# Performance work log

Measured on AMD Instinct MI355X. Metric: run time of the kernel, lower is better.

## Reference

```python
import jax, jax.numpy as jnp
import numpy as np
import math

# batch, in-channels, attention_maps, heads, features (== input height), frames
B, C, M, H, F_, W = 2, 8, 8, 8, 256, 512
HD = F_ // H  # head dim = 32


def conv2d(x, w, pad):
    return jax.lax.conv_general_dilated(x, w, (1, 1), pad,
                                        dimension_numbers=('NCHW', 'OIHW', 'NCHW'))


def rotary(x):
    # lucidrains-style interleaved rotary over last dim; x: [..., seq, d]
    d, seq = x.shape[-1], x.shape[-2]
    inv_freq = 1.0 / (10000.0 ** (jnp.arange(0, d, 2, dtype=jnp.float32) / d))
    freqs = jnp.arange(seq, dtype=jnp.float32)[:, None] * inv_freq[None, :]  # [seq, d/2]
    freqs = jnp.repeat(freqs, 2, axis=-1)  # [seq, d], each freq repeated for the (x1,x2) pair
    cos, sin = jnp.cos(freqs), jnp.sin(freqs)
    x1, x2 = x[..., 0::2], x[..., 1::2]
    xr = jnp.stack((-x2, x1), axis=-1).reshape(x.shape)  # rotate_half
    return x * cos + xr * sin


def setup_inputs() -> dict:
    key = jax.random.key(0)
    ks = jax.random.split(key, 12)
    s = 0.02
    return {
        'x': jax.random.normal(ks[0], (B, C, F_, W), jnp.float32),
        'prev_qk': jax.random.normal(ks[1], (B, M, H, W, W), jnp.float32) * 0.1,
        'q_c1': jax.random.normal(ks[2], (M, C, 3, 3), jnp.float32) * s,
        'q_lin': jax.random.normal(ks[3], (M, F_, F_), jnp.float32) * s,
        'q_c2': jax.random.normal(ks[4], (M, M, 1, 3), jnp.float32) * s,
        'k_c1': jax.random.normal(ks[5], (M, C, 3, 3), jnp.float32) * s,
        'k_lin': jax.random.normal(ks[6], (M, F_, F_), jnp.float32) * s,
        'k_c2': jax.random.normal(ks[7], (M, M, 1, 3), jnp.float32) * s,
        'v_c1': jax.random.normal(ks[8], (M, C, 3, 3), jnp.float32) * s,
        'v_lin': jax.random.normal(ks[9], (M, F_, F_), jnp.float32) * s,
        'v_c2': jax.random.normal(ks[10], (M, M, 1, 3), jnp.float32) * s,
        'o_w': jax.random.normal(ks[11], (M, F_, F_), jnp.float32) * s,
    }


def _proj(x, wc1, wl, wc2):
    h = conv2d(x, wc1, [(1, 1), (1, 1)])        # [B,M,F,W] 3x3 conv, no bias
    h = jnp.einsum('bcfw,cgf->bcgw', h, wl)      # MultichannelLinear: per-map linear on feature dim
    h = conv2d(h, wc2, [(0, 0), (1, 1)])         # (1,3) conv along frames
    return h


def _heads(t):
    # [B,M,F,W] -> transpose(2,3) -> [B,M,W,F] -> [B,M,W,H,HD] -> [B,M,H,W,HD]
    return t.transpose(0, 1, 3, 2).reshape(B, M, W, H, HD).transpose(0, 1, 3, 2, 4)


def reference(x, prev_qk, q_c1, q_lin, q_c2, k_c1, k_lin, k_c2, v_c1, v_lin, v_c2, o_w):
    q = rotary(_heads(_proj(x, q_c1, q_lin, q_c2)))
    k = rotary(_heads(_proj(x, k_c1, k_lin, k_c2)))
    v = _heads(_proj(x, v_c1, v_lin, v_c2))
    # scaled by sqrt(h) where h == input height == features (non-standard)
    qk = jnp.einsum('bmhqd,bmhkd->bmhqk', q, k) / math.sqrt(F_) + prev_qk
    a = jnp.einsum('bmhqk,bmhkd->bmhqd', jax.nn.softmax(qk, axis=-1), v)
    a = a.transpose(0, 1, 3, 2, 4).reshape(B, M, W, F_).transpose(0, 1, 3, 2)  # [B,M,F,W]
    out = jnp.einsum('bcfw,cgf->bcgw', a, o_w)  # o_proj MultichannelLinear
    return (out, qk)
```

## Files before the change

kernel.cpp:

```cpp
#include <hip/hip_runtime.h>

#define B 2
#define C 8
#define M 8
#define H 8
#define F 256
#define W 512
#define HD 32
#define MFF (M * F * F)

typedef __attribute__((ext_vector_type(8))) __bf16 bf16x8;
typedef __attribute__((ext_vector_type(4))) float f32x4;

__device__ __forceinline__ unsigned short f2bf(float f) {
    unsigned int u = __float_as_uint(f);
    return (unsigned short)((u + 0x7fffu + ((u >> 16) & 1u)) >> 16);
}

__device__ __forceinline__ unsigned int packsplit(float v) {
    unsigned short h = f2bf(v);
    float hf = __uint_as_float((unsigned int)h << 16);
    unsigned short lo = f2bf(v - hf);
    return (unsigned int)h | ((unsigned int)lo << 16);
}

__global__ __launch_bounds__(256) void wsplit_kernel(const float* __restrict__ w0,
                                                     const float* __restrict__ w1,
                                                     const float* __restrict__ w2,
                                                     const float* __restrict__ w3,
                                                     unsigned short* __restrict__ hi) {
    int idx = blockIdx.x * 256 + threadIdx.x;
    int set = idx >> 17;
    int off = (idx & 131071) * 4;
    const float* src = (set == 0) ? w0 : (set == 1) ? w1 : (set == 2) ? w2 : w3;
    float4 v = *(const float4*)&src[off];
    unsigned short* hp = hi + (size_t)set * MFF + off;
    unsigned short* lp = hp + 4 * MFF;
    ushort4 hv, lv;
    float x;
    x = v.x; hv.x = f2bf(x); lv.x = f2bf(x - __uint_as_float((unsigned)hv.x << 16));
    x = v.y; hv.y = f2bf(x); lv.y = f2bf(x - __uint_as_float((unsigned)hv.y << 16));
    x = v.z; hv.z = f2bf(x); lv.z = f2bf(x - __uint_as_float((unsigned)hv.z << 16));
    x = v.w; hv.w = f2bf(x); lv.w = f2bf(x - __uint_as_float((unsigned)hv.w << 16));
    *(ushort4*)hp = hv;
    *(ushort4*)lp = lv;
}

__global__ __launch_bounds__(256) void conv1_kernel(const float* __restrict__ x,
                                                    const float* __restrict__ w0,
                                                    const float* __restrict__ w1,
                                                    const float* __restrict__ w2,
                                                    unsigned int* __restrict__ out) {
    int t = threadIdx.x;
    int zb = blockIdx.z;
    int b = zb >> 3, m = zb & 7;
    int wi = blockIdx.x * 64 + (t & 63);
    int f0t = blockIdx.y * 32 + (t >> 6) * 8;
    const float* xb = x + (size_t)b * C * F * W;
    const float* wq = w0 + m * 72;
    const float* wk = w1 + m * 72;
    const float* wv = w2 + m * 72;
    int wm = (wi > 0) ? wi - 1 : 0;
    int wp = (wi < W - 1) ? wi + 1 : W - 1;
    bool e0 = (wi > 0), e1 = (wi < W - 1);
    float acc[3][8] = {};
    for (int i = 0; i < 8; ++i) {
        const float* xi = xb + (size_t)i * F * W;
        float v0[10], v1[10], v2[10];
        #pragma unroll
        for (int rr = 0; rr < 10; ++rr) {
            int ff = f0t + rr - 1;
            if (ff >= 0 && ff < F) {
                const float* xr = xi + (size_t)ff * W;
                float a = xr[wm], bb = xr[wi], c = xr[wp];
                v0[rr] = e0 ? a : 0.f;
                v1[rr] = bb;
                v2[rr] = e1 ? c : 0.f;
            } else {
                v0[rr] = 0.f; v1[rr] = 0.f; v2[rr] = 0.f;
            }
        }
        #pragma unroll
        for (int p = 0; p < 3; ++p) {
            const float* wt = ((p == 0) ? wq : (p == 1) ? wk : wv) + i * 9;
            #pragma unroll
            for (int df = 0; df < 3; ++df) {
                float s0 = wt[df * 3 + 0];
                float s1 = wt[df * 3 + 1];
                float s2 = wt[df * 3 + 2];
                #pragma unroll
                for (int ff = 0; ff < 8; ++ff)
                    acc[p][ff] += v0[ff + df] * s0 + v1[ff + df] * s1 + v2[ff + df] * s2;
            }
        }
    }
    #pragma unroll
    for (int p = 0; p < 3; ++p) {
        size_t zo = (size_t)(p * 16 + zb) * F;
        #pragma unroll
        for (int ff = 0; ff < 8; ++ff)
            out[(zo + f0t + ff) * W + wi] = packsplit(acc[p][ff]);
    }
}

__global__ __launch_bounds__(256) void lin_kernel(const unsigned int* __restrict__ in32,
                                                  const unsigned short* __restrict__ whA,
                                                  const unsigned short* __restrict__ whB,
                                                  const unsigned short* __restrict__ whC,
                                                  float* __restrict__ out) {
    __shared__ unsigned int BsH[64][20];
    __shared__ unsigned int BsL[64][20];
    int t = threadIdx.x;
    int z = blockIdx.z;
    int proj = z >> 4, m = z & 7;
    const unsigned short* wh = ((proj == 0) ? whA : (proj == 1) ? whB : whC) + (size_t)m * F * F;
    const unsigned short* wl = wh + 4 * MFF;
    const unsigned int* ib = in32 + (size_t)z * F * W;
    float* ob = out + (size_t)z * F * W;
    int g0 = blockIdx.y * 64, wb0 = blockIdx.x * 64;
    int wv = t >> 6, l = t & 63, lr = l & 15, lg = l >> 4;
    int wgr = wv >> 1, wgc = wv & 1;
    int sp = t & 15;
    int sg = t >> 4;

    uint4 ra, rb;
    ra = *(const uint4*)&ib[(size_t)(2 * sp) * W + wb0 + sg * 4];
    rb = *(const uint4*)&ib[(size_t)(2 * sp + 1) * W + wb0 + sg * 4];

    f32x4 acc[2][2];
    acc[0][0] = (f32x4)0.f; acc[0][1] = (f32x4)0.f;
    acc[1][0] = (f32x4)0.f; acc[1][1] = (f32x4)0.f;

    for (int s = 0; s < 8; ++s) {
        int f0 = s * 32;
        if (s) __syncthreads();
        unsigned int aw[4] = {ra.x, ra.y, ra.z, ra.w};
        unsigned int bw[4] = {rb.x, rb.y, rb.z, rb.w};
        #pragma unroll
        for (int j = 0; j < 4; ++j) {
            BsH[sg * 4 + j][sp] = (aw[j] & 0xFFFFu) | (bw[j] << 16);
            BsL[sg * 4 + j][sp] = (aw[j] >> 16) | (bw[j] & 0xFFFF0000u);
        }
        __syncthreads();
        if (s < 7) {
            ra = *(const uint4*)&ib[(size_t)(f0 + 32 + 2 * sp) * W + wb0 + sg * 4];
            rb = *(const uint4*)&ib[(size_t)(f0 + 32 + 2 * sp + 1) * W + wb0 + sg * 4];
        }
        bf16x8 ah[2], al[2], bh[2], bl[2];
        #pragma unroll
        for (int ti = 0; ti < 2; ++ti) {
            size_t ar = (size_t)(g0 + wgr * 32 + ti * 16 + lr) * F + f0 + lg * 8;
            ah[ti] = *(const bf16x8*)&wh[ar];
            al[ti] = *(const bf16x8*)&wl[ar];
        }
        #pragma unroll
        for (int tj = 0; tj < 2; ++tj) {
            int wc = wgc * 32 + tj * 16 + lr;
            bh[tj] = *(const bf16x8*)((const unsigned short*)&BsH[wc][0] + lg * 8);
            bl[tj] = *(const bf16x8*)((const unsigned short*)&BsL[wc][0] + lg * 8);
        }
        #pragma unroll
        for (int ti = 0; ti < 2; ++ti)
            #pragma unroll
            for (int tj = 0; tj < 2; ++tj) {
                acc[ti][tj] = __builtin_amdgcn_mfma_f32_16x16x32_bf16(ah[ti], bh[tj], acc[ti][tj], 0, 0, 0);
                acc[ti][tj] = __builtin_amdgcn_mfma_f32_16x16x32_bf16(ah[ti], bl[tj], acc[ti][tj], 0, 0, 0);
                acc[ti][tj] = __builtin_amdgcn_mfma_f32_16x16x32_bf16(al[ti], bh[tj], acc[ti][tj], 0, 0, 0);
            }
    }
    #pragma unroll
    for (int ti = 0; ti < 2; ++ti)
        #pragma unroll
        for (int tj = 0; tj < 2; ++tj)
            #pragma unroll
            for (int r = 0; r < 4; ++r) {
                int g = g0 + wgr * 32 + ti * 16 + lg * 4 + r;
                int w = wb0 + wgc * 32 + tj * 16 + lr;
                ob[(size_t)g * W + w] = acc[ti][tj][r];
            }
}

__global__ __launch_bounds__(256) void conv2_heads_kernel(const float* __restrict__ in,
                                                          const float* __restrict__ w0c,
                                                          const float* __restrict__ w1c,
                                                          const float* __restrict__ w2c,
                                                          unsigned short* __restrict__ outp) {
    __shared__ float wl[192];
    __shared__ float Ot[64][65];
    int t = threadIdx.x;
    int z = blockIdx.z;
    int proj = z >> 4, bz = z & 15;
    int b = bz >> 3, o = bz & 7;
    const float* wt = (proj == 0) ? w0c : (proj == 1) ? w1c : w2c;
    int do_rot = (proj < 2);
    if (t < 192) wl[t] = wt[t];
    __syncthreads();
    int f0 = blockIdx.y * 64, w0 = blockIdx.x * 64;
    const float* ib = in + ((size_t)proj * 16 + (size_t)b * M) * F * W;
    int wgi = t & 15, fr = t >> 4;
    int wq = w0 + wgi * 4;
    bool eL = (wq > 0);
    bool eR = (wq + 4 < W);
    #pragma unroll
    for (int fi = 0; fi < 4; ++fi) {
        int f = f0 + fr * 4 + fi;
        float a0 = 0.f, a1 = 0.f, a2 = 0.f, a3 = 0.f;
        #pragma unroll
        for (int i = 0; i < 8; ++i) {
            const float* r = ib + ((size_t)i * F + f) * W + wq;
            float4 v = *(const float4*)r;
            float vlft = eL ? r[-1] : 0.f;
            float vrgt = eR ? r[4] : 0.f;
            const float* wr = &wl[(o * 8 + i) * 3];
            float c0 = wr[0], c1 = wr[1], c2 = wr[2];
            a0 += vlft * c0 + v.x * c1 + v.y * c2;
            a1 += v.x  * c0 + v.y * c1 + v.z * c2;
            a2 += v.y  * c0 + v.z * c1 + v.w * c2;
            a3 += v.z  * c0 + v.w * c1 + vrgt * c2;
        }
        Ot[fr * 4 + fi][wgi * 4 + 0] = a0;
        Ot[fr * 4 + fi][wgi * 4 + 1] = a1;
        Ot[fr * 4 + fi][wgi * 4 + 2] = a2;
        Ot[fr * 4 + fi][wgi * 4 + 3] = a3;
    }
    __syncthreads();
    size_t zbase = (size_t)z * H * W * HD;
    if (do_rot) {
        for (int k = 0; k < 16; ++k) {
            int idx = k * 256 + t;
            int ddh = idx & 63;
            int wi = idx >> 6;
            int f = f0 + ddh;
            int h = f >> 5, d = f & 31;
            float e  = Ot[ddh & ~1][wi];
            float od = Ot[ddh | 1][wi];
            int jp = d >> 1;
            float invf = exp2f(-(float)jp * 0.83048202372184058f);
            float th = (float)(w0 + wi) * invf;
            float cs = __cosf(th), sn = __sinf(th);
            float val = (d & 1) ? (od * cs + e * sn) : (e * cs - od * sn);
            outp[zbase + ((size_t)h * W + (w0 + wi)) * HD + d] = f2bf(val);
        }
    } else {
        for (int k = 0; k < 16; ++k) {
            int idx = k * 256 + t;
            int wi = idx & 63;
            int ddh = idx >> 6;
            int f = f0 + ddh;
            int h = f >> 5, d = f & 31;
            outp[zbase + ((size_t)(h * HD + d)) * W + (w0 + wi)] = f2bf(Ot[ddh][wi]);
        }
    }
}

__global__ __launch_bounds__(256) void attn_kernel(const unsigned short* __restrict__ qb,
                                                   const unsigned short* __restrict__ kb,
                                                   const unsigned short* __restrict__ vtb,
                                                   const float* __restrict__ prev,
                                                   float* __restrict__ qk,
                                                   unsigned int* __restrict__ abuf) {
    __shared__ __align__(16) unsigned short PT[4][16 * 72];
    int t = threadIdx.x;
    int l = t & 63, wv = t >> 6;
    int lr = l & 15, lg = l >> 4;
    int w0 = blockIdx.x * 64;
    int bmh = blockIdx.y;
    const unsigned short* Q  = qb  + (size_t)bmh * W * HD;
    const unsigned short* K  = kb  + (size_t)bmh * W * HD;
    const unsigned short* VT = vtb + (size_t)bmh * HD * W;
    const float* P0 = prev + (size_t)bmh * W * W;
    float* QK = qk + (size_t)bmh * W * W;
    int bm = bmh >> 3, h = bmh & 7;
    unsigned int* A = abuf + ((size_t)bm * F + h * HD) * W;

    int qrow = w0 + wv * 16;
    bf16x8 qf = *(const bf16x8*)&Q[(size_t)(qrow + lr) * HD + lg * 8];

    float m_i[4], l_i[4];
    f32x4 accA[2];
    #pragma unroll
    for (int r = 0; r < 4; ++r) { m_i[r] = -3.0e38f; l_i[r] = 0.f; }
    accA[0] = (f32x4)0.f;
    accA[1] = (f32x4)0.f;

    bf16x8 kfA[4], kfB[4];
    f32x4 pvA[4], pvB[4];

    auto issue = [&](bf16x8 (&kf)[4], f32x4 (&pv)[4], int c) {
        int j0 = c * 64;
        #pragma unroll
        for (int ct = 0; ct < 4; ++ct)
            kf[ct] = *(const bf16x8*)&K[(size_t)(j0 + ct * 16 + lr) * HD + lg * 8];
        #pragma unroll
        for (int ct = 0; ct < 4; ++ct) {
            const float* pr = &P0[(size_t)(qrow + lg * 4) * W + j0 + ct * 16 + lr];
            #pragma unroll
            for (int r = 0; r < 4; ++r) pv[ct][r] = __builtin_nontemporal_load(&pr[(size_t)r * W]);
        }
    };

    auto step = [&](bf16x8 (&kf)[4], f32x4 (&pv)[4], int c) {
        int j0 = c * 64;
        f32x4 sc[4];
        #pragma unroll
        for (int ct = 0; ct < 4; ++ct)
            sc[ct] = __builtin_amdgcn_mfma_f32_16x16x32_bf16(qf, kf[ct], pv[ct] * 16.f, 0, 0, 0);
        bf16x8 vf[2][2];
        #pragma unroll
        for (int ks = 0; ks < 2; ++ks)
            #pragma unroll
            for (int ct2 = 0; ct2 < 2; ++ct2)
                vf[ks][ct2] = *(const bf16x8*)&VT[(size_t)(ct2 * 16 + lr) * W + j0 + ks * 32 + lg * 8];
        float sv[4][4];
        #pragma unroll
        for (int ct = 0; ct < 4; ++ct) {
            #pragma unroll
            for (int r = 0; r < 4; ++r) {
                sv[ct][r] = sc[ct][r] * 0.0625f;
                __builtin_nontemporal_store(sv[ct][r],
                    &QK[(size_t)(qrow + lg * 4 + r) * W + j0 + ct * 16 + lr]);
            }
        }
        float p[4][4];
        #pragma unroll
        for (int r = 0; r < 4; ++r) {
            float cm = fmaxf(fmaxf(sv[0][r], sv[1][r]), fmaxf(sv[2][r], sv[3][r]));
            #pragma unroll
            for (int off = 1; off < 16; off <<= 1) cm = fmaxf(cm, __shfl_xor(cm, off));
            float mn = fmaxf(m_i[r], cm);
            float alpha = __expf(m_i[r] - mn);
            m_i[r] = mn;
            float rs = 0.f;
            #pragma unroll
            for (int ct = 0; ct < 4; ++ct) { p[ct][r] = __expf(sv[ct][r] - mn); rs += p[ct][r]; }
            #pragma unroll
            for (int off = 1; off < 16; off <<= 1) rs += __shfl_xor(rs, off);
            l_i[r] = l_i[r] * alpha + rs;
            accA[0][r] *= alpha;
            accA[1][r] *= alpha;
        }
        unsigned short* PTw = &PT[wv][0];
        #pragma unroll
        for (int ct = 0; ct < 4; ++ct)
            #pragma unroll
            for (int r = 0; r < 4; ++r)
                PTw[(lg * 4 + r) * 72 + ct * 16 + lr] = f2bf(p[ct][r]);
        asm volatile("s_waitcnt lgkmcnt(0)" ::: "memory");
        __builtin_amdgcn_sched_barrier(0);
        bf16x8 pf[2];
        pf[0] = *(const bf16x8*)&PTw[lr * 72 + lg * 8];
        pf[1] = *(const bf16x8*)&PTw[lr * 72 + 32 + lg * 8];
        #pragma unroll
        for (int ks = 0; ks < 2; ++ks)
            #pragma unroll
            for (int ct2 = 0; ct2 < 2; ++ct2)
                accA[ct2] = __builtin_amdgcn_mfma_f32_16x16x32_bf16(pf[ks], vf[ks][ct2], accA[ct2], 0, 0, 0);
    };

    issue(kfA, pvA, 0);
    #pragma unroll
    for (int cc = 0; cc < 4; ++cc) {
        issue(kfB, pvB, 2 * cc + 1);
        step(kfA, pvA, 2 * cc);
        if (cc < 3) issue(kfA, pvA, 2 * cc + 2);
        step(kfB, pvB, 2 * cc + 1);
    }

    float inv[4];
    #pragma unroll
    for (int r = 0; r < 4; ++r) inv[r] = 1.f / l_i[r];
    float* Otf = (float*)&PT[wv][0];
    asm volatile("s_waitcnt lgkmcnt(0)" ::: "memory");
    #pragma unroll
    for (int ct2 = 0; ct2 < 2; ++ct2)
        #pragma unroll
        for (int r = 0; r < 4; ++r)
            Otf[(lg * 4 + r) * 33 + ct2 * 16 + lr] = accA[ct2][r] * inv[r];
    asm volatile("s_waitcnt lgkmcnt(0)" ::: "memory");
    __builtin_amdgcn_sched_barrier(0);
    #pragma unroll
    for (int k = 0; k < 8; ++k) {
        int flat = k * 64 + l;
        int woff = flat & 15, d = flat >> 4;
        A[(size_t)d * W + w0 + wv * 16 + woff] = packsplit(Otf[woff * 33 + d]);
    }
}

extern "C" void kernel_launch(void* const* d_in, const int* in_sizes, int n_in,
                              void* d_out, int out_size, void* d_ws, size_t ws_size,
                              hipStream_t stream) {
    const float* x    = (const float*)d_in[0];
    const float* prev = (const float*)d_in[1];
    const float* qc1  = (const float*)d_in[2];
    const float* qlin = (const float*)d_in[3];
    const float* qc2  = (const float*)d_in[4];
    const float* kc1  = (const float*)d_in[5];
    const float* klin = (const float*)d_in[6];
    const float* kc2  = (const float*)d_in[7];
    const float* vc1  = (const float*)d_in[8];
    const float* vlin = (const float*)d_in[9];
    const float* vc2  = (const float*)d_in[10];
    const float* ow   = (const float*)d_in[11];
    float* out0  = (float*)d_out;
    float* qkout = out0 + (size_t)B * M * F * W;
    float* ws = (float*)d_ws;
    size_t n = (size_t)B * M * F * W;
    float* r1 = ws;
    float* r2 = ws + 3 * n;
    unsigned int* r1u = (unsigned int*)r1;
    unsigned int* r2u = (unsigned int*)r2;
    unsigned short* qkv16 = (unsigned short*)r1;
    unsigned short* whi = (unsigned short*)(ws + 6 * n);

    dim3 blk(256);
    dim3 gsplit(2048), gconv1(8, 8, 16), glin3(8, 4, 48), gconv2(8, 4, 48);
    dim3 gattn(8, 128), glin1(8, 4, 16);

    wsplit_kernel<<<gsplit, blk, 0, stream>>>(qlin, klin, vlin, ow, whi);
    conv1_kernel<<<gconv1, blk, 0, stream>>>(x, qc1, kc1, vc1, r1u);
    lin_kernel<<<glin3, blk, 0, stream>>>(r1u, whi, whi + MFF, whi + 2 * MFF, r2);
    conv2_heads_kernel<<<gconv2, blk, 0, stream>>>(r2, qc2, kc2, vc2, qkv16);
    attn_kernel<<<gattn, blk, 0, stream>>>(qkv16, qkv16 + n, qkv16 + 2 * n, prev, qkout, r2u);
    lin_kernel<<<glin1, blk, 0, stream>>>(r2u, whi + 3 * MFF, whi + 3 * MFF, whi + 3 * MFF, out0);
}
```

Baseline: 414.2 us.

## Stage V tile in LDS, remap attention grid, drop nontemporal hints

```diff
diff --git a/kernel.cpp b/kernel.cpp
--- a/kernel.cpp
+++ b/kernel.cpp
@@ -259,12 +259,14 @@
                                                    const float* __restrict__ prev,
                                                    float* __restrict__ qk,
                                                    unsigned int* __restrict__ abuf) {
+    __shared__ __align__(16) unsigned short VsT[32 * 520];
     __shared__ __align__(16) unsigned short PT[4][16 * 72];
     int t = threadIdx.x;
     int l = t & 63, wv = t >> 6;
     int lr = l & 15, lg = l >> 4;
-    int w0 = blockIdx.x * 64;
-    int bmh = blockIdx.y;
+    int Lid = blockIdx.x;
+    int bmh = (Lid & 7) * 16 + ((Lid >> 3) & 15);
+    int w0 = (Lid >> 7) * 64;
     const unsigned short* Q  = qb  + (size_t)bmh * W * HD;
     const unsigned short* K  = kb  + (size_t)bmh * W * HD;
     const unsigned short* VT = vtb + (size_t)bmh * HD * W;
@@ -273,6 +275,12 @@
     int bm = bmh >> 3, h = bmh & 7;
     unsigned int* A = abuf + ((size_t)bm * F + h * HD) * W;
 
+    #pragma unroll
+    for (int it = 0; it < 8; ++it) {
+        int e16 = it * 256 + t;
+        int hd = e16 >> 6, w8 = (e16 & 63) * 8;
+        *(uint4*)&VsT[hd * 520 + w8] = *(const uint4*)&VT[(size_t)hd * W + w8];
+    }
     int qrow = w0 + wv * 16;
     bf16x8 qf = *(const bf16x8*)&Q[(size_t)(qrow + lr) * HD + lg * 8];
 
@@ -283,6 +291,8 @@
     accA[0] = (f32x4)0.f;
     accA[1] = (f32x4)0.f;
 
+    __syncthreads();
+
     bf16x8 kfA[4], kfB[4];
     f32x4 pvA[4], pvB[4];
 
@@ -295,7 +305,7 @@
         for (int ct = 0; ct < 4; ++ct) {
             const float* pr = &P0[(size_t)(qrow + lg * 4) * W + j0 + ct * 16 + lr];
             #pragma unroll
-            for (int r = 0; r < 4; ++r) pv[ct][r] = __builtin_nontemporal_load(&pr[(size_t)r * W]);
+            for (int r = 0; r < 4; ++r) pv[ct][r] = pr[(size_t)r * W];
         }
     };
 
@@ -305,20 +315,13 @@
         #pragma unroll
         for (int ct = 0; ct < 4; ++ct)
             sc[ct] = __builtin_amdgcn_mfma_f32_16x16x32_bf16(qf, kf[ct], pv[ct] * 16.f, 0, 0, 0);
-        bf16x8 vf[2][2];
-        #pragma unroll
-        for (int ks = 0; ks < 2; ++ks)
-            #pragma unroll
-            for (int ct2 = 0; ct2 < 2; ++ct2)
-                vf[ks][ct2] = *(const bf16x8*)&VT[(size_t)(ct2 * 16 + lr) * W + j0 + ks * 32 + lg * 8];
         float sv[4][4];
         #pragma unroll
         for (int ct = 0; ct < 4; ++ct) {
             #pragma unroll
             for (int r = 0; r < 4; ++r) {
                 sv[ct][r] = sc[ct][r] * 0.0625f;
-                __builtin_nontemporal_store(sv[ct][r],
-                    &QK[(size_t)(qrow + lg * 4 + r) * W + j0 + ct * 16 + lr]);
+                QK[(size_t)(qrow + lg * 4 + r) * W + j0 + ct * 16 + lr] = sv[ct][r];
             }
         }
         float p[4][4];
@@ -353,8 +356,10 @@
         #pragma unroll
         for (int ks = 0; ks < 2; ++ks)
             #pragma unroll
-            for (int ct2 = 0; ct2 < 2; ++ct2)
-                accA[ct2] = __builtin_amdgcn_mfma_f32_16x16x32_bf16(pf[ks], vf[ks][ct2], accA[ct2], 0, 0, 0);
+            for (int ct2 = 0; ct2 < 2; ++ct2) {
+                bf16x8 vf = *(const bf16x8*)&VsT[(ct2 * 16 + lr) * 520 + j0 + ks * 32 + lg * 8];
+                accA[ct2] = __builtin_amdgcn_mfma_f32_16x16x32_bf16(pf[ks], vf, accA[ct2], 0, 0, 0);
+            }
     };
 
     issue(kfA, pvA, 0);
@@ -414,7 +419,7 @@
 
     dim3 blk(256);
     dim3 gsplit(2048), gconv1(8, 8, 16), glin3(8, 4, 48), gconv2(8, 4, 48);
-    dim3 gattn(8, 128), glin1(8, 4, 16);
+    dim3 gattn(1024), glin1(8, 4, 16);
 
     wsplit_kernel<<<gsplit, blk, 0, stream>>>(qlin, klin, vlin, ow, whi);
     conv1_kernel<<<gconv1, blk, 0, stream>>>(x, qc1, kc1, vc1, r1u);
```

Result: faster. 404.2 us (-2.4%).
